# Performance work log

Hardware: AMD Instinct MI355X
Metric: run time of the kernel (lower is better)

## Reference

```python
import jax, jax.numpy as jnp
import numpy as np

N = 100000   # nodes
E = 640000   # edges
H = 8        # attention heads
C = 16       # hidden_channels (per-head out dim)
IN = 4       # in_channels
G = 64       # graphs in the batch
NE = 2       # num_experts
HC = H * C   # 128 = concat feature width
SLOPE = 0.2  # GATConv leaky_relu negative slope


def _p(k, shape):
    return 0.1 * jax.random.normal(k, shape, jnp.float32)


def setup_inputs() -> dict:
    key = jax.random.key(0)
    ks = jax.random.split(key, 32)
    inp = {
        "x": jax.random.normal(ks[0], (N, IN), jnp.float32),
        "edge_index": jax.random.randint(ks[1], (2, E), 0, N),
        "edge_attr": jax.random.normal(ks[2], (E, 1), jnp.float32),
        "batch": jnp.sort(jax.random.randint(ks[3], (N,), 0, G)),
    }
    i = 4
    for l, d in zip((1, 2, 3), (IN, HC, HC)):
        inp[f"w{l}"] = _p(ks[i], (d, HC)); i += 1      # node lin
        inp[f"as{l}"] = _p(ks[i], (H, C)); i += 1      # att_src
        inp[f"ad{l}"] = _p(ks[i], (H, C)); i += 1      # att_dst
        inp[f"we{l}"] = _p(ks[i], (1, HC)); i += 1     # lin_edge
        inp[f"ae{l}"] = _p(ks[i], (H, C)); i += 1      # att_edge
        inp[f"b{l}"] = jnp.zeros((HC,), jnp.float32)
    inp["fw1"] = _p(ks[i], (HC, 4 * C)); inp["fb1"] = jnp.zeros((4 * C,), jnp.float32)
    inp["fw2"] = _p(ks[i + 1], (4 * C, NE)); inp["fb2"] = jnp.zeros((NE,), jnp.float32)
    return inp


def gat_layer(x, src, dst, eattr, w, a_s, a_d, we, a_e, b):
    """PyG GATConv (concat=True, edge_dim=1): gather-attend-segment_softmax-scatter."""
    n = x.shape[0]
    h = (x @ w).reshape(n, H, C)                       # [N,H,C]
    alpha_src = jnp.sum(h * a_s, axis=-1)              # [N,H]
    alpha_dst = jnp.sum(h * a_d, axis=-1)              # [N,H]
    ef = (eattr @ we).reshape(-1, H, C)                # [E,H,C]
    alpha_e = jnp.sum(ef * a_e, axis=-1)               # [E,H]
    alpha = jax.nn.leaky_relu(alpha_src[src] + alpha_dst[dst] + alpha_e, SLOPE)
    # segment softmax over incoming edges of each dst node
    m = jax.lax.stop_gradient(jax.ops.segment_max(alpha, dst, num_segments=n))
    m = jnp.where(jnp.isfinite(m), m, 0.0)
    ex = jnp.exp(alpha - m[dst])
    den = jax.ops.segment_sum(ex, dst, num_segments=n)
    alpha = ex / (den[dst] + 1e-16)
    out = jax.ops.segment_sum(h[src] * alpha[:, :, None], dst, num_segments=n)
    return out.reshape(n, HC) + b


def add_self_loops_mean(src, dst, eattr, n):
    """add_self_loops(fill_value='mean'): self-loop attr = mean of incoming edge attrs."""
    cnt = jax.ops.segment_sum(jnp.ones(src.shape, eattr.dtype), dst, num_segments=n)
    loop = jax.ops.segment_sum(eattr, dst, num_segments=n) / jnp.maximum(cnt, 1.0)[:, None]
    idx = jnp.arange(n, dtype=src.dtype)
    return (jnp.concatenate([src, idx]), jnp.concatenate([dst, idx]),
            jnp.concatenate([eattr, loop], axis=0))


def reference(x, edge_index, edge_attr, batch,
              w1, as1, ad1, we1, ae1, b1,
              w2, as2, ad2, we2, ae2, b2,
              w3, as3, ad3, we3, ae3, b3,
              fw1, fb1, fw2, fb2):
    src, dst = edge_index[0], edge_index[1]
    # conv1: add_self_loops=False
    h = jax.nn.relu(gat_layer(x, src, dst, edge_attr, w1, as1, ad1, we1, ae1, b1))
    # conv2/conv3: default add_self_loops=True with fill_value='mean'
    s2, d2, e2 = add_self_loops_mean(src, dst, edge_attr, x.shape[0])
    h = jax.nn.relu(gat_layer(h, s2, d2, e2, w2, as2, ad2, we2, ae2, b2))
    h = jax.nn.relu(gat_layer(h, s2, d2, e2, w3, as3, ad3, we3, ae3, b3))
    # global mean pool over `batch`
    gsum = jax.ops.segment_sum(h, batch, num_segments=G)
    cnt = jax.ops.segment_sum(jnp.ones((h.shape[0],), h.dtype), batch, num_segments=G)
    emb = gsum / jnp.maximum(cnt, 1.0)[:, None]
    gh = jax.nn.relu(emb @ fw1 + fb1)
    return gh @ fw2 + fb2
```

## Files before the change

kernel.cpp:

```cpp
#include <hip/hip_runtime.h>
#include <hip/hip_bf16.h>
#include <math.h>

#define NHEAD 8
#define CDIM 16
#define HCDIM 128
#define NGRAPH 64
#define WEXT 144
#define SWPAD 136

typedef __attribute__((ext_vector_type(8))) short short8;
typedef __attribute__((ext_vector_type(4))) float f32x4;

static __device__ __forceinline__ unsigned short f2bf(float f) {
    unsigned u = __float_as_uint(f);
    unsigned r = (u + 0x7FFF + ((u >> 16) & 1)) >> 16;
    return (unsigned short)r;
}
static __device__ __forceinline__ float bf2f(unsigned short s) {
    return __uint_as_float(((unsigned)s) << 16);
}


__global__ void setup0(int* __restrict__ deg,
                       float* __restrict__ gsum,
                       const float* __restrict__ w2, const float* __restrict__ w3,
                       unsigned short* __restrict__ wt2, unsigned short* __restrict__ wt3,
                       const float* __restrict__ we1, const float* __restrict__ ae1,
                       const float* __restrict__ we2, const float* __restrict__ ae2,
                       const float* __restrict__ we3, const float* __restrict__ ae3,
                       float* __restrict__ kc,
                       const float* __restrict__ as2, const float* __restrict__ ad2,
                       const float* __restrict__ as3, const float* __restrict__ ad3,
                       const float* __restrict__ w1,
                       const float* __restrict__ as1, const float* __restrict__ ad1,
                       float* __restrict__ wastab, float* __restrict__ wadtab,
                       const int* __restrict__ batch, int* __restrict__ gstart, int n) {
    int i = blockIdx.x * 256 + threadIdx.x;
    if (i < n) deg[i] = 0;
    if (i < NGRAPH * HCDIM) gsum[i] = 0.f;
    if (i < WEXT * HCDIM) {
        int nn = i >> 7, k = i & 127;
        float v2, v3;
        if (nn < HCDIM) {
            v2 = w2[k * HCDIM + nn];
            v3 = w3[k * HCDIM + nn];
        } else if (nn < HCDIM + NHEAD) {
            int h = nn - HCDIM;
            float s2 = 0.f, s3 = 0.f;
#pragma unroll
            for (int c = 0; c < CDIM; ++c) {
                s2 += w2[k * HCDIM + h * CDIM + c] * as2[h * CDIM + c];
                s3 += w3[k * HCDIM + h * CDIM + c] * as3[h * CDIM + c];
            }
            v2 = s2; v3 = s3;
        } else {
            int h = nn - HCDIM - NHEAD;
            float s2 = 0.f, s3 = 0.f;
#pragma unroll
            for (int c = 0; c < CDIM; ++c) {
                s2 += w2[k * HCDIM + h * CDIM + c] * ad2[h * CDIM + c];
                s3 += w3[k * HCDIM + h * CDIM + c] * ad3[h * CDIM + c];
            }
            v2 = s2; v3 = s3;
        }
        wt2[nn * HCDIM + k] = f2bf(v2);
        wt3[nn * HCDIM + k] = f2bf(v3);
    }
    if (i < 24) {
        int l = i >> 3, h = i & 7;
        const float* we = (l == 0) ? we1 : ((l == 1) ? we2 : we3);
        const float* ae = (l == 0) ? ae1 : ((l == 1) ? ae2 : ae3);
        float s = 0.f;
        for (int c = 0; c < CDIM; ++c) s += we[h * CDIM + c] * ae[h * CDIM + c];
        kc[i] = s;
    }
    if (i >= 18560 && i <= 18560 + NGRAPH) {
        int g = i - 18560;
        int lo = 0, hi = n;
        while (lo < hi) {
            int mid = (lo + hi) >> 1;
            if (batch[mid] < g) lo = mid + 1; else hi = mid;
        }
        gstart[g] = lo;
    }
    if (i >= 18700 && i < 18732) {
        int t = i - 18700;
        int k = t >> 3, h = t & 7;
        float ss = 0.f, sd = 0.f;
#pragma unroll
        for (int c = 0; c < CDIM; ++c) {
            ss += w1[k * HCDIM + h * CDIM + c] * as1[h * CDIM + c];
            sd += w1[k * HCDIM + h * CDIM + c] * ad1[h * CDIM + c];
        }
        wastab[t] = ss;
        wadtab[t] = sd;
    }
}

__global__ void count_deg(const int* __restrict__ dst, int* __restrict__ deg,
                          int* __restrict__ erank, int E) {
    int e = blockIdx.x * 256 + threadIdx.x;
    if (e >= E) return;
    erank[e] = atomicAdd(&deg[dst[e]], 1);
}

__global__ __launch_bounds__(512) void block_sum(const int* __restrict__ deg,
                                                 int* __restrict__ bsum, int n) {
    __shared__ int s[512];
    int i = blockIdx.x * 512 + threadIdx.x;
    s[threadIdx.x] = (i < n) ? deg[i] : 0;
    __syncthreads();
    for (int off = 256; off > 0; off >>= 1) {
        if (threadIdx.x < off) s[threadIdx.x] += s[threadIdx.x + off];
        __syncthreads();
    }
    if (threadIdx.x == 0) bsum[blockIdx.x] = s[0];
}

__global__ __launch_bounds__(512) void scan_final2(const int* __restrict__ deg,
                                                   const int* __restrict__ bsum, int nb,
                                                   int* __restrict__ eoff, int n) {
    __shared__ int ls[512];
    __shared__ int s[512];
    const int t = threadIdx.x;
    ls[t] = (t < nb) ? bsum[t] : 0;
    int i = blockIdx.x * 512 + t;
    s[t] = (i < n) ? deg[i] : 0;
    __syncthreads();
    for (int off = 1; off < 512; off <<= 1) {
        int a1 = (t >= off) ? ls[t - off] : 0;
        int a2 = (t >= off) ? s[t - off] : 0;
        __syncthreads();
        ls[t] += a1; s[t] += a2;
        __syncthreads();
    }
    int base = (blockIdx.x > 0) ? ls[blockIdx.x - 1] : 0;
    if (i < n) eoff[i + 1] = base + s[t];
    if (i == 0) eoff[0] = 0;
}

__global__ void scatter_edges(const int* __restrict__ src, const int* __restrict__ dst,
                              const float* __restrict__ eattr,
                              const int* __restrict__ eoff,
                              const int* __restrict__ erank,
                              int2* __restrict__ epack, int E) {
    int e = blockIdx.x * 256 + threadIdx.x;
    if (e >= E) return;
    int p = eoff[dst[e]] + erank[e];
    epack[p] = make_int2(src[e], __float_as_int(eattr[e]));
}


__global__ __launch_bounds__(256) void gat_aggregate1(
    const float* __restrict__ x,
    const int2*  __restrict__ epack,
    const int*   __restrict__ eoff,
    const float* __restrict__ w1,
    const float* __restrict__ wastab,
    const float* __restrict__ wadtab,
    const float* __restrict__ kc,
    const float* __restrict__ bias,
    unsigned short* __restrict__ outbf,
    int n) {
    const int lane = threadIdx.x & 63;
    const int l16 = lane & 15;
    int nid = ((blockIdx.x * 256 + threadIdx.x) >> 6) * 4 + (lane >> 4);
    if (nid >= n) return;
    const int h = l16 >> 1;
    const int c0 = l16 * 8;

    float was0 = wastab[0 * NHEAD + h], was1_ = wastab[1 * NHEAD + h];
    float was2 = wastab[2 * NHEAD + h], was3 = wastab[3 * NHEAD + h];
    float wad0 = wadtab[0 * NHEAD + h], wad1_ = wadtab[1 * NHEAD + h];
    float wad2 = wadtab[2 * NHEAD + h], wad3 = wadtab[3 * NHEAD + h];

    float4 xd = *(const float4*)(x + (long)nid * 4);
    const float adst_h = xd.x * wad0 + xd.y * wad1_ + xd.z * wad2 + xd.w * wad3;
    const float k_h = kc[h];
    const int e0 = eoff[nid], e1 = eoff[nid + 1];

    float den = 0.f;
    float a0 = 0.f, a1 = 0.f, a2 = 0.f, a3 = 0.f;

    for (int base = e0; base < e1; base += 4) {
        int2 ep[4];
#pragma unroll
        for (int j = 0; j < 4; ++j) {
            int idx = base + j; idx = (idx < e1) ? idx : (e1 - 1);
            ep[j] = epack[idx];
        }
        float4 xs[4];
#pragma unroll
        for (int j = 0; j < 4; ++j) xs[j] = *(const float4*)(x + (long)ep[j].x * 4);
#pragma unroll
        for (int j = 0; j < 4; ++j) {
            bool valid = (base + j < e1);
            float as_e = xs[j].x * was0 + xs[j].y * was1_ + xs[j].z * was2 + xs[j].w * was3;
            float a = as_e + adst_h + __int_as_float(ep[j].y) * k_h;
            a = (a > 0.f) ? a : 0.2f * a;
            float w = valid ? __expf(a) : 0.f;
            den += w;
            a0 += xs[j].x * w; a1 += xs[j].y * w;
            a2 += xs[j].z * w; a3 += xs[j].w * w;
        }
    }

    float inv = 1.f / (den + 1e-16f);
    short8 o;
#pragma unroll
    for (int c = 0; c < 8; ++c) {
        float oc = a0 * w1[0 * HCDIM + c0 + c] + a1 * w1[1 * HCDIM + c0 + c] +
                   a2 * w1[2 * HCDIM + c0 + c] + a3 * w1[3 * HCDIM + c0 + c];
        oc = fmaxf(oc * inv + bias[c0 + c], 0.f);
        o[c] = (short)f2bf(oc);
    }
    *(short8*)(outbf + (long)nid * HCDIM + c0) = o;
}


__global__ __launch_bounds__(256) void gemm_mfma(const unsigned short* __restrict__ A,
                                                 const unsigned short* __restrict__ Wt,
                                                 unsigned short* __restrict__ Ybf,
                                                 float* __restrict__ asrcn,
                                                 float* __restrict__ adstn, int n) {
    __shared__ unsigned short sW[WEXT][SWPAD];
    for (int i = threadIdx.x; i < WEXT * 16; i += 256) {
        int r = i >> 4, c = (i & 15) << 3;
        *(short8*)&sW[r][c] = *(const short8*)(Wt + r * HCDIM + c);
    }
    __syncthreads();

    const int wave = threadIdx.x >> 6;
    const int lane = threadIdx.x & 63;
    const int quad = lane >> 4;
    const int l16  = lane & 15;
    const int rowbase = (blockIdx.x * 8 + wave * 2) * 16;

    f32x4 acc[2][9];
#pragma unroll
    for (int r = 0; r < 2; ++r)
#pragma unroll
        for (int t = 0; t < 9; ++t) acc[r][t] = (f32x4){0.f, 0.f, 0.f, 0.f};

#pragma unroll
    for (int kb = 0; kb < HCDIM; kb += 32) {
        short8 a[2];
#pragma unroll
        for (int r = 0; r < 2; ++r) {
            int row = rowbase + r * 16 + l16;
            row = (row < n) ? row : (n - 1);
            a[r] = *(const short8*)(A + (long)row * HCDIM + kb + quad * 8);
        }
#pragma unroll
        for (int nt = 0; nt < 9; ++nt) {
            short8 b = *(const short8*)(&sW[nt * 16 + l16][kb + quad * 8]);
#pragma unroll
            for (int r = 0; r < 2; ++r)
                acc[r][nt] = __builtin_amdgcn_mfma_f32_16x16x32_bf16(a[r], b, acc[r][nt], 0, 0, 0);
        }
    }

#pragma unroll
    for (int r = 0; r < 2; ++r) {
#pragma unroll
        for (int reg = 0; reg < 4; ++reg) {
            int row = rowbase + r * 16 + quad * 4 + reg;
            if (row < n) {
                unsigned short* yp = Ybf + (long)row * HCDIM + l16;
#pragma unroll
                for (int nt = 0; nt < 8; ++nt) yp[nt * 16] = f2bf(acc[r][nt][reg]);
                float cv = acc[r][8][reg];
                if (l16 < 8) asrcn[row * NHEAD + l16] = cv;
                else         adstn[row * NHEAD + (l16 - 8)] = cv;
            }
        }
    }
}


__global__ __launch_bounds__(256) void gat_aggregate(
    const unsigned short* __restrict__ hlin,
    const float* __restrict__ asrc,
    const float* __restrict__ adst,
    const int2*  __restrict__ epack,
    const int*   __restrict__ eoff,
    const float* __restrict__ kc,
    const float* __restrict__ bias,
    unsigned short* __restrict__ out,
    int n, int use_loop) {
    const int lane = threadIdx.x & 63;
    const int l16 = lane & 15;
    int nid = ((blockIdx.x * 256 + threadIdx.x) >> 6) * 4 + (lane >> 4);
    if (nid >= n) return;
    const int h = l16 >> 1;
    const int c0 = l16 * 8;

    const float adst_h = adst[nid * NHEAD + h];
    const float k_h = kc[h];
    const int e0 = eoff[nid], e1 = eoff[nid + 1];

    float den = 0.f, sume = 0.f;
    float acc[8];
#pragma unroll
    for (int c = 0; c < 8; ++c) acc[c] = 0.f;

    for (int base = e0; base < e1; base += 4) {
        int2 ep[4];
#pragma unroll
        for (int j = 0; j < 4; ++j) {
            int idx = base + j; idx = (idx < e1) ? idx : (e1 - 1);
            ep[j] = epack[idx];
        }
        float av[4]; short8 hv[4];
#pragma unroll
        for (int j = 0; j < 4; ++j) {
            av[j] = asrc[ep[j].x * NHEAD + h];
            hv[j] = *(const short8*)(hlin + (long)ep[j].x * HCDIM + c0);
        }
#pragma unroll
        for (int j = 0; j < 4; ++j) {
            bool valid = (base + j < e1);
            float ea = __int_as_float(ep[j].y);
            float a = av[j] + adst_h + ea * k_h;
            a = (a > 0.f) ? a : 0.2f * a;
            float w = valid ? __expf(a) : 0.f;
            sume += valid ? ea : 0.f;
            den += w;
#pragma unroll
            for (int c = 0; c < 8; ++c)
                acc[c] += bf2f((unsigned short)hv[j][c]) * w;
        }
    }

    if (use_loop) {
        float fl = sume / fmaxf((float)(e1 - e0), 1.f);
        float a = asrc[nid * NHEAD + h] + adst_h + fl * k_h;
        a = (a > 0.f) ? a : 0.2f * a;
        float w = __expf(a);
        short8 hv = *(const short8*)(hlin + (long)nid * HCDIM + c0);
        den += w;
#pragma unroll
        for (int c = 0; c < 8; ++c)
            acc[c] += bf2f((unsigned short)hv[c]) * w;
    }

    float inv = 1.f / (den + 1e-16f);
    short8 o;
#pragma unroll
    for (int c = 0; c < 8; ++c) {
        float oc = fmaxf(acc[c] * inv + bias[c0 + c], 0.f);
        o[c] = (short)f2bf(oc);
    }
    *(short8*)(out + (long)nid * HCDIM + c0) = o;
}


__global__ __launch_bounds__(128) void pool_seg(const unsigned short* __restrict__ H,
                                                const int* __restrict__ gstart,
                                                float* __restrict__ gsum) {
    const int c = threadIdx.x;
    const int g = blockIdx.x >> 3;
    const int chunk = blockIdx.x & 7;
    int s0 = gstart[g], s1 = gstart[g + 1];
    int len = s1 - s0;
    if (len <= 0) return;
    int cl = (len + 7) >> 3;
    int i0 = s0 + chunk * cl;
    int i1 = min(i0 + cl, s1);
    if (i0 >= i1) return;
    float acc = 0.f;
    int i = i0;
    for (; i + 4 <= i1; i += 4) {
        float v0 = bf2f(H[(long)i * HCDIM + c]);
        float v1 = bf2f(H[(long)(i + 1) * HCDIM + c]);
        float v2 = bf2f(H[(long)(i + 2) * HCDIM + c]);
        float v3 = bf2f(H[(long)(i + 3) * HCDIM + c]);
        acc += (v0 + v1) + (v2 + v3);
    }
    for (; i < i1; ++i) acc += bf2f(H[(long)i * HCDIM + c]);
    atomicAdd(&gsum[g * HCDIM + c], acc);
}

__global__ __launch_bounds__(64) void mlp_kernel(const float* __restrict__ gsum,
                                                 const int* __restrict__ gstart,
                                                 const float* __restrict__ fw1,
                                                 const float* __restrict__ fb1,
                                                 const float* __restrict__ fw2,
                                                 const float* __restrict__ fb2,
                                                 float* __restrict__ out) {
    const int g = blockIdx.x;
    const int j = threadIdx.x;
    __shared__ float emb[HCDIM];
    __shared__ float gh[64];
    int cnt = gstart[g + 1] - gstart[g];
    float invc = 1.f / fmaxf((float)cnt, 1.f);
    emb[j] = gsum[g * HCDIM + j] * invc;
    emb[j + 64] = gsum[g * HCDIM + 64 + j] * invc;
    __syncthreads();
    float a = fb1[j];
    for (int k = 0; k < HCDIM; ++k) a += emb[k] * fw1[k * 64 + j];
    gh[j] = fmaxf(a, 0.f);
    __syncthreads();
    if (j < 2) {
        float o = fb2[j];
        for (int k = 0; k < 64; ++k) o += gh[k] * fw2[k * 2 + j];
        out[g * 2 + j] = o;
    }
}


extern "C" void kernel_launch(void* const* d_in, const int* in_sizes, int n_in,
                              void* d_out, int out_size, void* d_ws, size_t ws_size,
                              hipStream_t stream) {
    const float* x     = (const float*)d_in[0];
    const int*   eidx  = (const int*)d_in[1];
    const float* eattr = (const float*)d_in[2];
    const int*   batch = (const int*)d_in[3];
    const float* w1  = (const float*)d_in[4];
    const float* as1 = (const float*)d_in[5];
    const float* ad1 = (const float*)d_in[6];
    const float* we1 = (const float*)d_in[7];
    const float* ae1 = (const float*)d_in[8];
    const float* b1  = (const float*)d_in[9];
    const float* w2  = (const float*)d_in[10];
    const float* as2 = (const float*)d_in[11];
    const float* ad2 = (const float*)d_in[12];
    const float* we2 = (const float*)d_in[13];
    const float* ae2 = (const float*)d_in[14];
    const float* b2  = (const float*)d_in[15];
    const float* w3  = (const float*)d_in[16];
    const float* as3 = (const float*)d_in[17];
    const float* ad3 = (const float*)d_in[18];
    const float* we3 = (const float*)d_in[19];
    const float* ae3 = (const float*)d_in[20];
    const float* b3  = (const float*)d_in[21];
    const float* fw1 = (const float*)d_in[22];
    const float* fb1 = (const float*)d_in[23];
    const float* fw2 = (const float*)d_in[24];
    const float* fb2 = (const float*)d_in[25];

    const int N = in_sizes[3];
    const int E = in_sizes[2];
    const int* src = eidx;
    const int* dst = eidx + E;

    char* p = (char*)d_ws;
    auto alloc = [&](size_t bytes) {
        void* r = (void*)p;
        p += (bytes + 255) & ~(size_t)255;
        return r;
    };
    unsigned short* Abf = (unsigned short*)alloc((size_t)N * HCDIM * 2);
    unsigned short* Bbf = (unsigned short*)alloc((size_t)N * HCDIM * 2);
    float* asrcA  = (float*)alloc((size_t)N * NHEAD * 4);
    float* adstA  = (float*)alloc((size_t)N * NHEAD * 4);
    float* asrcB  = (float*)alloc((size_t)N * NHEAD * 4);
    float* adstB  = (float*)alloc((size_t)N * NHEAD * 4);
    int*   deg    = (int*)alloc((size_t)N * 4);
    int*   eoff   = (int*)alloc((size_t)(N + 1) * 4);
    int*   erank  = (int*)alloc((size_t)E * 4);
    int2*  epack  = (int2*)alloc((size_t)E * 8);
    int*   bsum   = (int*)alloc(((size_t)(N + 511) / 512) * 4);
    float* kc     = (float*)alloc(24 * 4);
    int*   gstart = (int*)alloc((NGRAPH + 1) * 4);
    float* gsum   = (float*)alloc(NGRAPH * HCDIM * 4);
    float* wastab = (float*)alloc(32 * 4);
    float* wadtab = (float*)alloc(32 * 4);
    unsigned short* wt2 = (unsigned short*)alloc(WEXT * HCDIM * 2);
    unsigned short* wt3 = (unsigned short*)alloc(WEXT * HCDIM * 2);

    const int NB = (N + 255) / 256;
    const int NB512 = (N + 511) / 512;
    const int EB = (E + 255) / 256;
    const int AGG_BLOCKS = (((N + 3) / 4) * 64 + 255) / 256;
    const int GEMM_BLOCKS = (N + 127) / 128;

    setup0<<<NB, 256, 0, stream>>>(deg, gsum,
                                   w2, w3, wt2, wt3,
                                   we1, ae1, we2, ae2, we3, ae3, kc,
                                   as2, ad2, as3, ad3,
                                   w1, as1, ad1, wastab, wadtab,
                                   batch, gstart, N);
    count_deg<<<EB, 256, 0, stream>>>(dst, deg, erank, E);
    block_sum<<<NB512, 512, 0, stream>>>(deg, bsum, N);
    scan_final2<<<NB512, 512, 0, stream>>>(deg, bsum, NB512, eoff, N);
    scatter_edges<<<EB, 256, 0, stream>>>(src, dst, eattr, eoff, erank, epack, E);

    gat_aggregate1<<<AGG_BLOCKS, 256, 0, stream>>>(x, epack, eoff, w1, wastab, wadtab,
                                                   kc + 0, b1, Bbf, N);
    gemm_mfma<<<GEMM_BLOCKS, 256, 0, stream>>>(Bbf, wt2, Abf, asrcB, adstB, N);
    gat_aggregate<<<AGG_BLOCKS, 256, 0, stream>>>(Abf, asrcB, adstB, epack, eoff,
                                                  kc + 8, b2, Bbf, N, 1);
    gemm_mfma<<<GEMM_BLOCKS, 256, 0, stream>>>(Bbf, wt3, Abf, asrcA, adstA, N);
    gat_aggregate<<<AGG_BLOCKS, 256, 0, stream>>>(Abf, asrcA, adstA, epack, eoff,
                                                  kc + 16, b3, Bbf, N, 1);

    pool_seg<<<NGRAPH * 8, 128, 0, stream>>>(Bbf, gstart, gsum);
    mlp_kernel<<<NGRAPH, 64, 0, stream>>>(gsum, gstart, fw1, fb1, fw2, fb2, (float*)d_out);
}
```

Before: 326.2 us.

## Fuse mean pooling with MLP head and prefetch GEMM A fragments

```diff
diff --git a/kernel.cpp b/kernel.cpp
--- a/kernel.cpp
+++ b/kernel.cpp
@@ -23,7 +23,6 @@
 
 
 __global__ void setup0(int* __restrict__ deg,
-                       float* __restrict__ gsum,
                        const float* __restrict__ w2, const float* __restrict__ w3,
                        unsigned short* __restrict__ wt2, unsigned short* __restrict__ wt3,
                        const float* __restrict__ we1, const float* __restrict__ ae1,
@@ -38,7 +37,6 @@
                        const int* __restrict__ batch, int* __restrict__ gstart, int n) {
     int i = blockIdx.x * 256 + threadIdx.x;
     if (i < n) deg[i] = 0;
-    if (i < NGRAPH * HCDIM) gsum[i] = 0.f;
     if (i < WEXT * HCDIM) {
         int nn = i >> 7, k = i & 127;
         float v2, v3;
@@ -237,20 +235,31 @@
     const int l16  = lane & 15;
     const int rowbase = (blockIdx.x * 8 + wave * 2) * 16;
 
+    long arow[2];
+#pragma unroll
+    for (int r = 0; r < 2; ++r) {
+        int row = rowbase + r * 16 + l16;
+        row = (row < n) ? row : (n - 1);
+        arow[r] = (long)row * HCDIM + quad * 8;
+    }
+
     f32x4 acc[2][9];
 #pragma unroll
     for (int r = 0; r < 2; ++r)
 #pragma unroll
         for (int t = 0; t < 9; ++t) acc[r][t] = (f32x4){0.f, 0.f, 0.f, 0.f};
 
+    short8 a[2];
+#pragma unroll
+    for (int r = 0; r < 2; ++r) a[r] = *(const short8*)(A + arow[r]);
+
 #pragma unroll
     for (int kb = 0; kb < HCDIM; kb += 32) {
-        short8 a[2];
-#pragma unroll
-        for (int r = 0; r < 2; ++r) {
-            int row = rowbase + r * 16 + l16;
-            row = (row < n) ? row : (n - 1);
-            a[r] = *(const short8*)(A + (long)row * HCDIM + kb + quad * 8);
+        short8 an[2];
+        if (kb + 32 < HCDIM) {
+#pragma unroll
+            for (int r = 0; r < 2; ++r)
+                an[r] = *(const short8*)(A + arow[r] + kb + 32);
         }
 #pragma unroll
         for (int nt = 0; nt < 9; ++nt) {
@@ -258,6 +267,10 @@
 #pragma unroll
             for (int r = 0; r < 2; ++r)
                 acc[r][nt] = __builtin_amdgcn_mfma_f32_16x16x32_bf16(a[r], b, acc[r][nt], 0, 0, 0);
+        }
+        if (kb + 32 < HCDIM) {
+#pragma unroll
+            for (int r = 0; r < 2; ++r) a[r] = an[r];
         }
     }
 
@@ -356,51 +369,47 @@
 }
 
 
-__global__ __launch_bounds__(128) void pool_seg(const unsigned short* __restrict__ H,
+__global__ __launch_bounds__(256) void pool_mlp(const unsigned short* __restrict__ H,
                                                 const int* __restrict__ gstart,
-                                                float* __restrict__ gsum) {
-    const int c = threadIdx.x;
-    const int g = blockIdx.x >> 3;
-    const int chunk = blockIdx.x & 7;
-    int s0 = gstart[g], s1 = gstart[g + 1];
-    int len = s1 - s0;
-    if (len <= 0) return;
-    int cl = (len + 7) >> 3;
-    int i0 = s0 + chunk * cl;
-    int i1 = min(i0 + cl, s1);
-    if (i0 >= i1) return;
+                                                const float* __restrict__ fw1,
+                                                const float* __restrict__ fb1,
+                                                const float* __restrict__ fw2,
+                                                const float* __restrict__ fb2,
+                                                float* __restrict__ out) {
+    const int g = blockIdx.x;
+    const int c = threadIdx.x & 127;
+    const int half = threadIdx.x >> 7;
+    const int s0 = gstart[g], s1 = gstart[g + 1];
+    const int cnt = s1 - s0;
+
     float acc = 0.f;
-    int i = i0;
-    for (; i + 4 <= i1; i += 4) {
+    int i = s0 + half;
+    for (; i + 6 < s1; i += 8) {
         float v0 = bf2f(H[(long)i * HCDIM + c]);
-        float v1 = bf2f(H[(long)(i + 1) * HCDIM + c]);
-        float v2 = bf2f(H[(long)(i + 2) * HCDIM + c]);
-        float v3 = bf2f(H[(long)(i + 3) * HCDIM + c]);
+        float v1 = bf2f(H[(long)(i + 2) * HCDIM + c]);
+        float v2 = bf2f(H[(long)(i + 4) * HCDIM + c]);
+        float v3 = bf2f(H[(long)(i + 6) * HCDIM + c]);
         acc += (v0 + v1) + (v2 + v3);
     }
-    for (; i < i1; ++i) acc += bf2f(H[(long)i * HCDIM + c]);
-    atomicAdd(&gsum[g * HCDIM + c], acc);
-}
-
-__global__ __launch_bounds__(64) void mlp_kernel(const float* __restrict__ gsum,
-                                                 const int* __restrict__ gstart,
-                                                 const float* __restrict__ fw1,
-                                                 const float* __restrict__ fb1,
-                                                 const float* __restrict__ fw2,
-                                                 const float* __restrict__ fb2,
-                                                 float* __restrict__ out) {
-    const int g = blockIdx.x;
-    const int j = threadIdx.x;
+    for (; i < s1; i += 2) acc += bf2f(H[(long)i * HCDIM + c]);
+
+    __shared__ float part[2][HCDIM];
     __shared__ float emb[HCDIM];
     __shared__ float gh[64];
-    int cnt = gstart[g + 1] - gstart[g];
-    float invc = 1.f / fmaxf((float)cnt, 1.f);
-    emb[j] = gsum[g * HCDIM + j] * invc;
-    emb[j + 64] = gsum[g * HCDIM + 64 + j] * invc;
+    part[half][c] = acc;
     __syncthreads();
-    float a = fb1[j];
-    for (int k = 0; k < HCDIM; ++k) a += emb[k] * fw1[k * 64 + j];
-    gh[j] = fmaxf(a, 0.f);
+    if (half == 0) {
+        float invc = 1.f / fmaxf((float)cnt, 1.f);
+        emb[c] = (part[0][c] + part[1][c]) * invc;
+    }
+    __syncthreads();
+    const int j = threadIdx.x;
+    if (j < 64) {
+        float a = fb1[j];
+#pragma unroll 4
+        for (int k = 0; k < HCDIM; ++k) a += emb[k] * fw1[k * 64 + j];
+        gh[j] = fmaxf(a, 0.f);
+    }
     __syncthreads();
     if (j < 2) {
         float o = fb2[j];
@@ -464,7 +473,6 @@
     int*   bsum   = (int*)alloc(((size_t)(N + 511) / 512) * 4);
     float* kc     = (float*)alloc(24 * 4);
     int*   gstart = (int*)alloc((NGRAPH + 1) * 4);
-    float* gsum   = (float*)alloc(NGRAPH * HCDIM * 4);
     float* wastab = (float*)alloc(32 * 4);
     float* wadtab = (float*)alloc(32 * 4);
     unsigned short* wt2 = (unsigned short*)alloc(WEXT * HCDIM * 2);
@@ -476,7 +484,7 @@
     const int AGG_BLOCKS = (((N + 3) / 4) * 64 + 255) / 256;
     const int GEMM_BLOCKS = (N + 127) / 128;
 
-    setup0<<<NB, 256, 0, stream>>>(deg, gsum,
+    setup0<<<NB, 256, 0, stream>>>(deg,
                                    w2, w3, wt2, wt3,
                                    we1, ae1, we2, ae2, we3, ae3, kc,
                                    as2, ad2, as3, ad3,
@@ -496,6 +504,5 @@
     gat_aggregate<<<AGG_BLOCKS, 256, 0, stream>>>(Abf, asrcA, adstA, epack, eoff,
                                                   kc + 16, b3, Bbf, N, 1);
 
-    pool_seg<<<NGRAPH * 8, 128, 0, stream>>>(Bbf, gstart, gsum);
-    mlp_kernel<<<NGRAPH, 64, 0, stream>>>(gsum, gstart, fw1, fb1, fw2, fb2, (float*)d_out);
-}
+    pool_mlp<<<NGRAPH, 256, 0, stream>>>(Bbf, gstart, fw1, fb1, fw2, fb2, (float*)d_out);
+}
```

After: 374.0 us. 1.15x slower.
